# Kernel optimization log

Measured on AMD Instinct MI355X. Metric: run time of the kernel, lower is better.

Reference implementation:

```python
import jax, jax.numpy as jnp
import numpy as np

D_MODEL = 1024
N_HEADS = 16
D_K = D_MODEL // N_HEADS
B, S = 2, 2048


def setup_inputs() -> dict:
    key = jax.random.key(0)
    ks = jax.random.split(key, 5)
    x = jax.random.normal(ks[0], (B, S, D_MODEL), dtype=jnp.float32)
    # causal 0/1 mask, broadcastable over batch and heads
    mask = jnp.tril(jnp.ones((S, S), dtype=jnp.int32))[None, None, :, :]
    scale = 1.0 / np.sqrt(D_MODEL)
    w_qkv_w = jax.random.normal(ks[1], (3 * D_MODEL, D_MODEL), dtype=jnp.float32) * scale
    w_qkv_b = jnp.zeros((3 * D_MODEL,), dtype=jnp.float32)
    w_o_w = jax.random.normal(ks[2], (D_MODEL, D_MODEL), dtype=jnp.float32) * scale
    w_o_b = jnp.zeros((D_MODEL,), dtype=jnp.float32)
    return {"x": x, "mask": mask, "w_qkv_w": w_qkv_w, "w_qkv_b": w_qkv_b,
            "w_o_w": w_o_w, "w_o_b": w_o_b}


def reference(x, mask, w_qkv_w, w_qkv_b, w_o_w, w_o_b):
    b, s, d = x.shape
    qkv = x @ w_qkv_w.T + w_qkv_b                       # [b, s, 3d]
    q, k, v = jnp.split(qkv, 3, axis=-1)
    # [b, h, s, dk]
    q = q.reshape(b, s, N_HEADS, D_K).transpose(0, 2, 1, 3)
    k = k.reshape(b, s, N_HEADS, D_K).transpose(0, 2, 1, 3)
    v = v.reshape(b, s, N_HEADS, D_K).transpose(0, 2, 1, 3)
    scores = jnp.einsum('bhqd,bhkd->bhqk', q, k) / jnp.sqrt(jnp.float32(D_K))
    scores = jnp.where(mask == 0, jnp.float32(-1e9), scores)
    attn = jax.nn.softmax(scores, axis=-1)
    out = jnp.einsum('bhqk,bhkd->bhqd', attn, v)        # [b, h, s, dk]
    out = out.transpose(0, 2, 1, 3).reshape(b, s, d)
    return out @ w_o_w.T + w_o_b
```

## Files before the change

### kernel.cpp

```cpp
#include <hip/hip_runtime.h>
#include <cstdint>
#include <cstddef>


typedef __attribute__((ext_vector_type(8))) short bf16x8;
typedef __attribute__((ext_vector_type(4))) float f32x4;
typedef __attribute__((ext_vector_type(4))) unsigned int u32x4;
typedef __attribute__((ext_vector_type(4))) unsigned short u16x4;
typedef __attribute__((ext_vector_type(8))) unsigned short u16x8;

__device__ __forceinline__ unsigned short f2b(float f) {
  unsigned int u = __float_as_uint(f);
  u = u + 0x7FFFu + ((u >> 16) & 1u);
  return (unsigned short)(u >> 16);
}
__device__ __forceinline__ unsigned short f2b_trunc(float f) {
  return (unsigned short)(__float_as_uint(f) >> 16);
}

__device__ __forceinline__ void gl_lds16(const unsigned short* g, unsigned short* s) {
  __builtin_amdgcn_global_load_lds((const __attribute__((address_space(1))) void*)g,
                                   (__attribute__((address_space(3))) void*)s, 16, 0, 0);
}

__global__ __launch_bounds__(256) void cvt_all(const float* __restrict__ x,
                                               const float* __restrict__ wq,
                                               const float* __restrict__ wo,
                                               unsigned short* __restrict__ xb,
                                               unsigned short* __restrict__ wqb,
                                               unsigned short* __restrict__ wob) {
  const int bid = blockIdx.x;
  const float* in;
  unsigned short* out;
  int base;
  if (bid < 4096)      { in = x;  out = xb;  base = bid; }
  else if (bid < 7168) { in = wq; out = wqb; base = bid - 4096; }
  else                 { in = wo; out = wob; base = bid - 7168; }
  const int idx = (base * 256 + threadIdx.x) * 4;
  f32x4 v = *(const f32x4*)(in + idx);
  u16x4 r;
  r[0] = f2b(v[0]); r[1] = f2b(v[1]); r[2] = f2b(v[2]); r[3] = f2b(v[3]);
  *(u16x4*)(out + idx) = r;
}

__global__ __launch_bounds__(256) void gemm_bt(const unsigned short* __restrict__ A,
                                               const unsigned short* __restrict__ W,
                                               const float* __restrict__ bias,
                                               unsigned short* __restrict__ Cb,
                                               int M, int N, int K, int qcols) {
  __shared__ unsigned short As[2][128 * 32];
  __shared__ unsigned short Bs[2][128 * 32];
  const int tid  = threadIdx.x;
  const int lane = tid & 63;
  const int w    = tid >> 6;
  const int wy   = w >> 1, wx = w & 1;
  const int l15  = lane & 15, quad = lane >> 4;
  const int xr2  = (l15 >> 1) & 3;
  const int m0 = blockIdx.y * 128, n0 = blockIdx.x * 128;

  const unsigned short* gA[2];
  const unsigned short* gB[2];
  int off[2];
#pragma unroll
  for (int p = 0; p < 2; ++p) {
    const int c = tid + p * 256;
    const int r = c >> 2;
    const int srcc = (c & 3) ^ ((r >> 1) & 3);
    gA[p] = A + (size_t)(m0 + r) * K + srcc * 8;
    gB[p] = W + (size_t)(n0 + r) * K + srcc * 8;
    off[p] = c * 8;
  }

  f32x4 acc[4][4];
#pragma unroll
  for (int i = 0; i < 4; ++i)
#pragma unroll
    for (int j = 0; j < 4; ++j) acc[i][j] = (f32x4){0.f, 0.f, 0.f, 0.f};

#pragma unroll
  for (int p = 0; p < 2; ++p) {
    gl_lds16(gA[p], &As[0][off[p]]);
    gl_lds16(gB[p], &Bs[0][off[p]]);
  }

  const int NIT = K >> 5;
  for (int it = 0; it < NIT; ++it) {
    __syncthreads();
    const int cur = it & 1;
    if (it + 1 < NIT) {
      const int kt = (it + 1) << 5;
#pragma unroll
      for (int p = 0; p < 2; ++p) {
        gl_lds16(gA[p] + kt, &As[cur ^ 1][off[p]]);
        gl_lds16(gB[p] + kt, &Bs[cur ^ 1][off[p]]);
      }
    }
    const unsigned short* Ac = As[cur];
    const unsigned short* Bc = Bs[cur];
    bf16x8 af[4], bfr[4];
#pragma unroll
    for (int i = 0; i < 4; ++i)
      af[i] = *(const bf16x8*)&Ac[(wy * 64 + i * 16 + l15) * 32 + (quad ^ xr2) * 8];
#pragma unroll
    for (int j = 0; j < 4; ++j)
      bfr[j] = *(const bf16x8*)&Bc[(wx * 64 + j * 16 + l15) * 32 + (quad ^ xr2) * 8];
#pragma unroll
    for (int i = 0; i < 4; ++i)
#pragma unroll
      for (int j = 0; j < 4; ++j)
        acc[i][j] = __builtin_amdgcn_mfma_f32_16x16x32_bf16(af[i], bfr[j], acc[i][j], 0, 0, 0);
  }

#pragma unroll
  for (int i = 0; i < 4; ++i) {
    const int row = m0 + wy * 64 + i * 16 + quad * 4;
#pragma unroll
    for (int j = 0; j < 4; ++j) {
      const int col = n0 + wx * 64 + j * 16 + l15;
      const float bv = bias[col];
      const float sc = (col < qcols) ? 0.125f : 1.0f;
#pragma unroll
      for (int r = 0; r < 4; ++r)
        Cb[(size_t)(row + r) * N + col] = f2b((acc[i][j][r] + bv) * sc);
    }
  }
}

__global__ __launch_bounds__(256) void gemm_bt64(const unsigned short* __restrict__ A,
                                                 const unsigned short* __restrict__ W,
                                                 const float* __restrict__ bias,
                                                 float* __restrict__ Cf,
                                                 int M, int N, int K) {
  __shared__ unsigned short As[2][64 * 32];
  __shared__ unsigned short Bs[2][128 * 32];
  const int tid  = threadIdx.x;
  const int lane = tid & 63;
  const int w    = tid >> 6;
  const int wy   = w >> 1, wx = w & 1;
  const int l15  = lane & 15, quad = lane >> 4;
  const int xr2  = (l15 >> 1) & 3;
  const int m0 = blockIdx.y * 64, n0 = blockIdx.x * 128;

  const unsigned short* gA0;
  int offA0;
  {
    const int c = tid;
    const int r = c >> 2;
    const int srcc = (c & 3) ^ ((r >> 1) & 3);
    gA0 = A + (size_t)(m0 + r) * K + srcc * 8;
    offA0 = c * 8;
  }
  const unsigned short* gB[2];
  int offB[2];
#pragma unroll
  for (int p = 0; p < 2; ++p) {
    const int c = tid + p * 256;
    const int r = c >> 2;
    const int srcc = (c & 3) ^ ((r >> 1) & 3);
    gB[p] = W + (size_t)(n0 + r) * K + srcc * 8;
    offB[p] = c * 8;
  }

  f32x4 acc[2][4];
#pragma unroll
  for (int i = 0; i < 2; ++i)
#pragma unroll
    for (int j = 0; j < 4; ++j) acc[i][j] = (f32x4){0.f, 0.f, 0.f, 0.f};

  gl_lds16(gA0, &As[0][offA0]);
#pragma unroll
  for (int p = 0; p < 2; ++p) gl_lds16(gB[p], &Bs[0][offB[p]]);

  const int NIT = K >> 5;
  for (int it = 0; it < NIT; ++it) {
    __syncthreads();
    const int cur = it & 1;
    if (it + 1 < NIT) {
      const int kt = (it + 1) << 5;
      gl_lds16(gA0 + kt, &As[cur ^ 1][offA0]);
#pragma unroll
      for (int p = 0; p < 2; ++p) gl_lds16(gB[p] + kt, &Bs[cur ^ 1][offB[p]]);
    }
    const unsigned short* Ac = As[cur];
    const unsigned short* Bc = Bs[cur];
    bf16x8 af[2], bfr[4];
#pragma unroll
    for (int i = 0; i < 2; ++i)
      af[i] = *(const bf16x8*)&Ac[(wy * 32 + i * 16 + l15) * 32 + (quad ^ xr2) * 8];
#pragma unroll
    for (int j = 0; j < 4; ++j)
      bfr[j] = *(const bf16x8*)&Bc[(wx * 64 + j * 16 + l15) * 32 + (quad ^ xr2) * 8];
#pragma unroll
    for (int i = 0; i < 2; ++i)
#pragma unroll
      for (int j = 0; j < 4; ++j)
        acc[i][j] = __builtin_amdgcn_mfma_f32_16x16x32_bf16(af[i], bfr[j], acc[i][j], 0, 0, 0);
  }

#pragma unroll
  for (int i = 0; i < 2; ++i) {
    const int row = m0 + wy * 32 + i * 16 + quad * 4;
#pragma unroll
    for (int j = 0; j < 4; ++j) {
      const int col = n0 + wx * 64 + j * 16 + l15;
      const float bv = bias[col];
#pragma unroll
      for (int r = 0; r < 4; ++r)
        Cf[(size_t)(row + r) * N + col] = acc[i][j][r] + bv;
    }
  }
}

__global__ __launch_bounds__(256) void transpose_v(const unsigned short* __restrict__ qkv,
                                                   unsigned short* __restrict__ vt) {
  __shared__ unsigned short tile[64][72];
  const int tid = threadIdx.x;
  const int bh = blockIdx.y, b = bh >> 4, h = bh & 15;
  const int s0 = blockIdx.x * 64;
  const int i = tid >> 2;
  const int j = (tid & 3) * 16;
  const unsigned short* g = qkv + (size_t)(b * 2048 + s0 + i) * 3072 + 2048 + h * 64 + j;
  *(u32x4*)&tile[i][j]     = *(const u32x4*)g;
  *(u32x4*)&tile[i][j + 8] = *(const u32x4*)(g + 8);
  __syncthreads();
  const int d  = tid >> 2;
  const int sj = (tid & 3) * 16;
  u16x8 o0, o1;
#pragma unroll
  for (int k = 0; k < 8; ++k) { o0[k] = tile[sj + k][d]; o1[k] = tile[sj + 8 + k][d]; }
  unsigned short* gout = vt + (size_t)(bh * 64 + d) * 2048 + s0 + sj;
  *(u16x8*)gout       = o0;
  *(u16x8*)(gout + 8) = o1;
}

__global__ __launch_bounds__(256, 3) void attn_fwd(const unsigned short* __restrict__ qkv,
                                                   const unsigned short* __restrict__ vt,
                                                   unsigned short* __restrict__ o) {
  __shared__ unsigned short Ks[2][64 * 72];
  __shared__ unsigned short Vs[2][64 * 72];
  __shared__ unsigned short pbuf[4][16 * 72];
  const int tid  = threadIdx.x;
  const int lane = tid & 63;
  const int w    = tid >> 6;
  const int l15  = lane & 15, quad = lane >> 4;
  const int bh = blockIdx.x, b = bh >> 4, h = bh & 15;
  const int qt = 15 - (int)blockIdx.y;
  const int q0 = qt * 128;
  const int qa = q0 + w * 32;
  const int qb = qa + 16;
  const int T = 2 * qt + 2;

  const int srow = tid >> 2;
  const int scol = (tid & 3) * 16;
  const unsigned short* gK = qkv + (size_t)(b * 2048 + srow) * 3072 + 1024 + h * 64 + scol;
  const unsigned short* gV = vt + (size_t)(bh * 64 + srow) * 2048 + scol;

  const unsigned short* qra = qkv + (size_t)(b * 2048 + qa + l15) * 3072 + h * 64;
  const unsigned short* qrb = qkv + (size_t)(b * 2048 + qb + l15) * 3072 + h * 64;
  const bf16x8 bq[2][2] = {
    { *(const bf16x8*)(qra + quad * 8), *(const bf16x8*)(qra + 32 + quad * 8) },
    { *(const bf16x8*)(qrb + quad * 8), *(const bf16x8*)(qrb + 32 + quad * 8) } };

  bf16x8 vones;
#pragma unroll
  for (int k = 0; k < 8; ++k) vones[k] = (short)0x3F80;

  f32x4 acc[2][4];
#pragma unroll
  for (int i = 0; i < 2; ++i)
#pragma unroll
    for (int j = 0; j < 4; ++j) acc[i][j] = (f32x4){0.f, 0.f, 0.f, 0.f};
  f32x4 accL[2] = {(f32x4){0.f, 0.f, 0.f, 0.f}, (f32x4){0.f, 0.f, 0.f, 0.f}};

  unsigned short* P = pbuf[w];

  {
    u32x4 k0 = *(const u32x4*)gK, k1 = *(const u32x4*)(gK + 8);
    u32x4 v0 = *(const u32x4*)gV, v1 = *(const u32x4*)(gV + 8);
    unsigned short* sK = &Ks[0][srow * 72 + scol];
    unsigned short* sV = &Vs[0][srow * 72 + scol];
    *(u32x4*)sK = k0; *(u32x4*)(sK + 8) = k1;
    *(u32x4*)sV = v0; *(u32x4*)(sV + 8) = v1;
  }

  for (int t = 0; t < T; ++t) {
    __syncthreads();
    const int cur = t & 1;
    const unsigned short* Kc = Ks[cur];
    const unsigned short* Vc = Vs[cur];
    u32x4 nk0, nk1, nv0, nv1;
    const bool more = (t + 1 < T);
    if (more) {
      const size_t ko = (size_t)(t + 1) * 64 * 3072;
      const int vo = (t + 1) * 64;
      nk0 = *(const u32x4*)(gK + ko); nk1 = *(const u32x4*)(gK + ko + 8);
      nv0 = *(const u32x4*)(gV + vo); nv1 = *(const u32x4*)(gV + vo + 8);
    }
    const int kv0 = t * 64;

    f32x4 st[2][4];
#pragma unroll
    for (int n = 0; n < 4; ++n) {
      const bf16x8 kA0 = *(const bf16x8*)&Kc[(n * 16 + l15) * 72 + quad * 8];
      const bf16x8 kA1 = *(const bf16x8*)&Kc[(n * 16 + l15) * 72 + 32 + quad * 8];
      f32x4 z0 = (f32x4){0.f, 0.f, 0.f, 0.f};
      z0 = __builtin_amdgcn_mfma_f32_16x16x32_bf16(kA0, bq[0][0], z0, 0, 0, 0);
      z0 = __builtin_amdgcn_mfma_f32_16x16x32_bf16(kA1, bq[0][1], z0, 0, 0, 0);
      st[0][n] = z0;
      f32x4 z1 = (f32x4){0.f, 0.f, 0.f, 0.f};
      z1 = __builtin_amdgcn_mfma_f32_16x16x32_bf16(kA0, bq[1][0], z1, 0, 0, 0);
      z1 = __builtin_amdgcn_mfma_f32_16x16x32_bf16(kA1, bq[1][1], z1, 0, 0, 0);
      st[1][n] = z1;
    }
    bf16x8 av[4][2];
#pragma unroll
    for (int j = 0; j < 4; ++j) {
      av[j][0] = *(const bf16x8*)&Vc[(j * 16 + l15) * 72 + quad * 8];
      av[j][1] = *(const bf16x8*)&Vc[(j * 16 + l15) * 72 + 32 + quad * 8];
    }
#pragma unroll
    for (int tq = 0; tq < 2; ++tq) {
      const int qbase = tq ? qb : qa;
      if (kv0 + 63 > qbase) {
        const int qrow = qbase + l15;
#pragma unroll
        for (int n = 0; n < 4; ++n)
#pragma unroll
          for (int r = 0; r < 4; ++r)
            if (kv0 + n * 16 + quad * 4 + r > qrow) st[tq][n][r] = -1e30f;
      }
#pragma unroll
      for (int n = 0; n < 4; ++n) {
#pragma unroll
        for (int r = 0; r < 4; ++r) st[tq][n][r] = __expf(st[tq][n][r]);
        u16x4 pw;
        pw[0] = f2b_trunc(st[tq][n][0]); pw[1] = f2b_trunc(st[tq][n][1]);
        pw[2] = f2b_trunc(st[tq][n][2]); pw[3] = f2b_trunc(st[tq][n][3]);
        *(u16x4*)&P[l15 * 72 + n * 16 + quad * 4] = pw;
      }
      const bf16x8 bp0 = *(const bf16x8*)&P[l15 * 72 + quad * 8];
      const bf16x8 bp1 = *(const bf16x8*)&P[l15 * 72 + 32 + quad * 8];
      accL[tq] = __builtin_amdgcn_mfma_f32_16x16x32_bf16(vones, bp0, accL[tq], 0, 0, 0);
      accL[tq] = __builtin_amdgcn_mfma_f32_16x16x32_bf16(vones, bp1, accL[tq], 0, 0, 0);
#pragma unroll
      for (int j = 0; j < 4; ++j) {
        acc[tq][j] = __builtin_amdgcn_mfma_f32_16x16x32_bf16(av[j][0], bp0, acc[tq][j], 0, 0, 0);
        acc[tq][j] = __builtin_amdgcn_mfma_f32_16x16x32_bf16(av[j][1], bp1, acc[tq][j], 0, 0, 0);
      }
    }
    if (more) {
      unsigned short* sK = &Ks[cur ^ 1][srow * 72 + scol];
      unsigned short* sV = &Vs[cur ^ 1][srow * 72 + scol];
      *(u32x4*)sK = nk0; *(u32x4*)(sK + 8) = nk1;
      *(u32x4*)sV = nv0; *(u32x4*)(sV + 8) = nv1;
    }
  }
#pragma unroll
  for (int tq = 0; tq < 2; ++tq) {
    const int qrow = (tq ? qb : qa) + l15;
    const float inv = 1.0f / accL[tq][0];
    unsigned short* orow = o + (size_t)(b * 2048 + qrow) * 1024 + h * 64;
#pragma unroll
    for (int j = 0; j < 4; ++j) {
      u16x4 ov;
      ov[0] = f2b(acc[tq][j][0] * inv); ov[1] = f2b(acc[tq][j][1] * inv);
      ov[2] = f2b(acc[tq][j][2] * inv); ov[3] = f2b(acc[tq][j][3] * inv);
      *(u16x4*)(orow + j * 16 + quad * 4) = ov;
    }
  }
}

extern "C" void kernel_launch(void* const* d_in, const int* in_sizes, int n_in,
                              void* d_out, int out_size, void* d_ws, size_t ws_size,
                              hipStream_t stream) {
  const float* x       = (const float*)d_in[0];
  const float* w_qkv_w = (const float*)d_in[2];
  const float* w_qkv_b = (const float*)d_in[3];
  const float* w_o_w   = (const float*)d_in[4];
  const float* w_o_b   = (const float*)d_in[5];
  float* out = (float*)d_out;

  unsigned short* ws    = (unsigned short*)d_ws;
  unsigned short* xb    = ws;
  unsigned short* wqb   = xb   + (size_t)4096 * 1024;
  unsigned short* wob   = wqb  + (size_t)3072 * 1024;
  unsigned short* qkvb  = wob  + (size_t)1024 * 1024;
  unsigned short* vtb   = qkvb + (size_t)4096 * 3072;
  unsigned short* attnb = vtb  + (size_t)2048 * 2048;

  cvt_all<<<8192, 256, 0, stream>>>(x, w_qkv_w, w_o_w, xb, wqb, wob);
  gemm_bt<<<dim3(24, 32), 256, 0, stream>>>(xb, wqb, w_qkv_b, qkvb, 4096, 3072, 1024, 1024);
  transpose_v<<<dim3(32, 32), 256, 0, stream>>>(qkvb, vtb);
  attn_fwd<<<dim3(32, 16), 256, 0, stream>>>(qkvb, vtb, attnb);
  gemm_bt64<<<dim3(8, 64), 256, 0, stream>>>(attnb, wob, w_o_b, out, 4096, 1024, 1024);
}
```

Measured before the change: 196.3 us.

## Halve attention and output GEMM tile sizes, load V directly from global

The attention kernel now gives each block 64 query rows (16 per wave) instead of 128, doubling the grid to 1024 blocks and raising the occupancy hint to 4. V fragments are read straight from global memory each iteration instead of being staged through double-buffered LDS, which frees LDS and registers. The output-projection GEMM tile shrinks from 64x128 to 64x64 to double its block count. The goal is better CU utilisation and load balance across the causal triangle, at the cost of less K reuse per block and uncached-through-LDS global V loads sitting on the critical path.

```diff
diff --git a/kernel.cpp b/kernel.cpp
--- a/kernel.cpp
+++ b/kernel.cpp
@@ -132,44 +132,35 @@
                                                  float* __restrict__ Cf,
                                                  int M, int N, int K) {
   __shared__ unsigned short As[2][64 * 32];
-  __shared__ unsigned short Bs[2][128 * 32];
+  __shared__ unsigned short Bs[2][64 * 32];
   const int tid  = threadIdx.x;
   const int lane = tid & 63;
   const int w    = tid >> 6;
   const int wy   = w >> 1, wx = w & 1;
   const int l15  = lane & 15, quad = lane >> 4;
   const int xr2  = (l15 >> 1) & 3;
-  const int m0 = blockIdx.y * 64, n0 = blockIdx.x * 128;
+  const int m0 = blockIdx.y * 64, n0 = blockIdx.x * 64;
 
   const unsigned short* gA0;
-  int offA0;
+  const unsigned short* gB0;
+  int off0;
   {
     const int c = tid;
     const int r = c >> 2;
     const int srcc = (c & 3) ^ ((r >> 1) & 3);
     gA0 = A + (size_t)(m0 + r) * K + srcc * 8;
-    offA0 = c * 8;
-  }
-  const unsigned short* gB[2];
-  int offB[2];
-#pragma unroll
-  for (int p = 0; p < 2; ++p) {
-    const int c = tid + p * 256;
-    const int r = c >> 2;
-    const int srcc = (c & 3) ^ ((r >> 1) & 3);
-    gB[p] = W + (size_t)(n0 + r) * K + srcc * 8;
-    offB[p] = c * 8;
-  }
-
-  f32x4 acc[2][4];
+    gB0 = W + (size_t)(n0 + r) * K + srcc * 8;
+    off0 = c * 8;
+  }
+
+  f32x4 acc[2][2];
 #pragma unroll
   for (int i = 0; i < 2; ++i)
 #pragma unroll
-    for (int j = 0; j < 4; ++j) acc[i][j] = (f32x4){0.f, 0.f, 0.f, 0.f};
-
-  gl_lds16(gA0, &As[0][offA0]);
-#pragma unroll
-  for (int p = 0; p < 2; ++p) gl_lds16(gB[p], &Bs[0][offB[p]]);
+    for (int j = 0; j < 2; ++j) acc[i][j] = (f32x4){0.f, 0.f, 0.f, 0.f};
+
+  gl_lds16(gA0, &As[0][off0]);
+  gl_lds16(gB0, &Bs[0][off0]);
 
   const int NIT = K >> 5;
   for (int it = 0; it < NIT; ++it) {
@@ -177,23 +168,22 @@
     const int cur = it & 1;
     if (it + 1 < NIT) {
       const int kt = (it + 1) << 5;
-      gl_lds16(gA0 + kt, &As[cur ^ 1][offA0]);
-#pragma unroll
-      for (int p = 0; p < 2; ++p) gl_lds16(gB[p] + kt, &Bs[cur ^ 1][offB[p]]);
+      gl_lds16(gA0 + kt, &As[cur ^ 1][off0]);
+      gl_lds16(gB0 + kt, &Bs[cur ^ 1][off0]);
     }
     const unsigned short* Ac = As[cur];
     const unsigned short* Bc = Bs[cur];
-    bf16x8 af[2], bfr[4];
+    bf16x8 af[2], bfr[2];
 #pragma unroll
     for (int i = 0; i < 2; ++i)
       af[i] = *(const bf16x8*)&Ac[(wy * 32 + i * 16 + l15) * 32 + (quad ^ xr2) * 8];
 #pragma unroll
-    for (int j = 0; j < 4; ++j)
-      bfr[j] = *(const bf16x8*)&Bc[(wx * 64 + j * 16 + l15) * 32 + (quad ^ xr2) * 8];
+    for (int j = 0; j < 2; ++j)
+      bfr[j] = *(const bf16x8*)&Bc[(wx * 32 + j * 16 + l15) * 32 + (quad ^ xr2) * 8];
 #pragma unroll
     for (int i = 0; i < 2; ++i)
 #pragma unroll
-      for (int j = 0; j < 4; ++j)
+      for (int j = 0; j < 2; ++j)
         acc[i][j] = __builtin_amdgcn_mfma_f32_16x16x32_bf16(af[i], bfr[j], acc[i][j], 0, 0, 0);
   }
 
@@ -201,8 +191,8 @@
   for (int i = 0; i < 2; ++i) {
     const int row = m0 + wy * 32 + i * 16 + quad * 4;
 #pragma unroll
-    for (int j = 0; j < 4; ++j) {
-      const int col = n0 + wx * 64 + j * 16 + l15;
+    for (int j = 0; j < 2; ++j) {
+      const int col = n0 + wx * 32 + j * 16 + l15;
       const float bv = bias[col];
 #pragma unroll
       for (int r = 0; r < 4; ++r)
@@ -233,140 +223,114 @@
   *(u16x8*)(gout + 8) = o1;
 }
 
-__global__ __launch_bounds__(256, 3) void attn_fwd(const unsigned short* __restrict__ qkv,
+__global__ __launch_bounds__(256, 4) void attn_fwd(const unsigned short* __restrict__ qkv,
                                                    const unsigned short* __restrict__ vt,
                                                    unsigned short* __restrict__ o) {
   __shared__ unsigned short Ks[2][64 * 72];
-  __shared__ unsigned short Vs[2][64 * 72];
   __shared__ unsigned short pbuf[4][16 * 72];
   const int tid  = threadIdx.x;
   const int lane = tid & 63;
   const int w    = tid >> 6;
   const int l15  = lane & 15, quad = lane >> 4;
   const int bh = blockIdx.x, b = bh >> 4, h = bh & 15;
-  const int qt = 15 - (int)blockIdx.y;
-  const int q0 = qt * 128;
-  const int qa = q0 + w * 32;
-  const int qb = qa + 16;
-  const int T = 2 * qt + 2;
+  const int qt = 31 - (int)blockIdx.y;
+  const int q0 = qt * 64 + w * 16;
+  const int T = qt + 1;
 
   const int srow = tid >> 2;
   const int scol = (tid & 3) * 16;
   const unsigned short* gK = qkv + (size_t)(b * 2048 + srow) * 3072 + 1024 + h * 64 + scol;
-  const unsigned short* gV = vt + (size_t)(bh * 64 + srow) * 2048 + scol;
-
-  const unsigned short* qra = qkv + (size_t)(b * 2048 + qa + l15) * 3072 + h * 64;
-  const unsigned short* qrb = qkv + (size_t)(b * 2048 + qb + l15) * 3072 + h * 64;
-  const bf16x8 bq[2][2] = {
-    { *(const bf16x8*)(qra + quad * 8), *(const bf16x8*)(qra + 32 + quad * 8) },
-    { *(const bf16x8*)(qrb + quad * 8), *(const bf16x8*)(qrb + 32 + quad * 8) } };
+  const unsigned short* gV = vt + (size_t)(bh * 64) * 2048;
+
+  const unsigned short* qr = qkv + (size_t)(b * 2048 + q0 + l15) * 3072 + h * 64;
+  const bf16x8 bq0 = *(const bf16x8*)(qr + quad * 8);
+  const bf16x8 bq1 = *(const bf16x8*)(qr + 32 + quad * 8);
 
   bf16x8 vones;
 #pragma unroll
   for (int k = 0; k < 8; ++k) vones[k] = (short)0x3F80;
 
-  f32x4 acc[2][4];
-#pragma unroll
-  for (int i = 0; i < 2; ++i)
-#pragma unroll
-    for (int j = 0; j < 4; ++j) acc[i][j] = (f32x4){0.f, 0.f, 0.f, 0.f};
-  f32x4 accL[2] = {(f32x4){0.f, 0.f, 0.f, 0.f}, (f32x4){0.f, 0.f, 0.f, 0.f}};
+  f32x4 acc[4];
+#pragma unroll
+  for (int j = 0; j < 4; ++j) acc[j] = (f32x4){0.f, 0.f, 0.f, 0.f};
+  f32x4 accL = (f32x4){0.f, 0.f, 0.f, 0.f};
 
   unsigned short* P = pbuf[w];
 
   {
     u32x4 k0 = *(const u32x4*)gK, k1 = *(const u32x4*)(gK + 8);
-    u32x4 v0 = *(const u32x4*)gV, v1 = *(const u32x4*)(gV + 8);
     unsigned short* sK = &Ks[0][srow * 72 + scol];
-    unsigned short* sV = &Vs[0][srow * 72 + scol];
     *(u32x4*)sK = k0; *(u32x4*)(sK + 8) = k1;
-    *(u32x4*)sV = v0; *(u32x4*)(sV + 8) = v1;
   }
 
   for (int t = 0; t < T; ++t) {
     __syncthreads();
     const int cur = t & 1;
     const unsigned short* Kc = Ks[cur];
-    const unsigned short* Vc = Vs[cur];
-    u32x4 nk0, nk1, nv0, nv1;
+    const int kv0 = t * 64;
+    bf16x8 av[4][2];
+#pragma unroll
+    for (int j = 0; j < 4; ++j) {
+      const unsigned short* vrow = gV + (size_t)(j * 16 + l15) * 2048 + kv0;
+      av[j][0] = *(const bf16x8*)(vrow + quad * 8);
+      av[j][1] = *(const bf16x8*)(vrow + 32 + quad * 8);
+    }
+    u32x4 nk0, nk1;
     const bool more = (t + 1 < T);
     if (more) {
       const size_t ko = (size_t)(t + 1) * 64 * 3072;
-      const int vo = (t + 1) * 64;
       nk0 = *(const u32x4*)(gK + ko); nk1 = *(const u32x4*)(gK + ko + 8);
-      nv0 = *(const u32x4*)(gV + vo); nv1 = *(const u32x4*)(gV + vo + 8);
-    }
-    const int kv0 = t * 64;
-
-    f32x4 st[2][4];
+    }
+    f32x4 st[4];
 #pragma unroll
     for (int n = 0; n < 4; ++n) {
       const bf16x8 kA0 = *(const bf16x8*)&Kc[(n * 16 + l15) * 72 + quad * 8];
       const bf16x8 kA1 = *(const bf16x8*)&Kc[(n * 16 + l15) * 72 + 32 + quad * 8];
-      f32x4 z0 = (f32x4){0.f, 0.f, 0.f, 0.f};
-      z0 = __builtin_amdgcn_mfma_f32_16x16x32_bf16(kA0, bq[0][0], z0, 0, 0, 0);
-      z0 = __builtin_amdgcn_mfma_f32_16x16x32_bf16(kA1, bq[0][1], z0, 0, 0, 0);
-      st[0][n] = z0;
-      f32x4 z1 = (f32x4){0.f, 0.f, 0.f, 0.f};
-      z1 = __builtin_amdgcn_mfma_f32_16x16x32_bf16(kA0, bq[1][0], z1, 0, 0, 0);
-      z1 = __builtin_amdgcn_mfma_f32_16x16x32_bf16(kA1, bq[1][1], z1, 0, 0, 0);
-      st[1][n] = z1;
-    }
-    bf16x8 av[4][2];
+      f32x4 z = (f32x4){0.f, 0.f, 0.f, 0.f};
+      z = __builtin_amdgcn_mfma_f32_16x16x32_bf16(kA0, bq0, z, 0, 0, 0);
+      z = __builtin_amdgcn_mfma_f32_16x16x32_bf16(kA1, bq1, z, 0, 0, 0);
+      st[n] = z;
+    }
+    if (kv0 + 63 > q0) {
+      const int qrow = q0 + l15;
+#pragma unroll
+      for (int n = 0; n < 4; ++n)
+#pragma unroll
+        for (int r = 0; r < 4; ++r)
+          if (kv0 + n * 16 + quad * 4 + r > qrow) st[n][r] = -1e30f;
+    }
+#pragma unroll
+    for (int n = 0; n < 4; ++n) {
+#pragma unroll
+      for (int r = 0; r < 4; ++r) st[n][r] = __expf(st[n][r]);
+      u16x4 pw;
+      pw[0] = f2b_trunc(st[n][0]); pw[1] = f2b_trunc(st[n][1]);
+      pw[2] = f2b_trunc(st[n][2]); pw[3] = f2b_trunc(st[n][3]);
+      *(u16x4*)&P[l15 * 72 + n * 16 + quad * 4] = pw;
+    }
+    const bf16x8 bp0 = *(const bf16x8*)&P[l15 * 72 + quad * 8];
+    const bf16x8 bp1 = *(const bf16x8*)&P[l15 * 72 + 32 + quad * 8];
+    accL = __builtin_amdgcn_mfma_f32_16x16x32_bf16(vones, bp0, accL, 0, 0, 0);
+    accL = __builtin_amdgcn_mfma_f32_16x16x32_bf16(vones, bp1, accL, 0, 0, 0);
 #pragma unroll
     for (int j = 0; j < 4; ++j) {
-      av[j][0] = *(const bf16x8*)&Vc[(j * 16 + l15) * 72 + quad * 8];
-      av[j][1] = *(const bf16x8*)&Vc[(j * 16 + l15) * 72 + 32 + quad * 8];
-    }
-#pragma unroll
-    for (int tq = 0; tq < 2; ++tq) {
-      const int qbase = tq ? qb : qa;
-      if (kv0 + 63 > qbase) {
-        const int qrow = qbase + l15;
-#pragma unroll
-        for (int n = 0; n < 4; ++n)
-#pragma unroll
-          for (int r = 0; r < 4; ++r)
-            if (kv0 + n * 16 + quad * 4 + r > qrow) st[tq][n][r] = -1e30f;
-      }
-#pragma unroll
-      for (int n = 0; n < 4; ++n) {
-#pragma unroll
-        for (int r = 0; r < 4; ++r) st[tq][n][r] = __expf(st[tq][n][r]);
-        u16x4 pw;
-        pw[0] = f2b_trunc(st[tq][n][0]); pw[1] = f2b_trunc(st[tq][n][1]);
-        pw[2] = f2b_trunc(st[tq][n][2]); pw[3] = f2b_trunc(st[tq][n][3]);
-        *(u16x4*)&P[l15 * 72 + n * 16 + quad * 4] = pw;
-      }
-      const bf16x8 bp0 = *(const bf16x8*)&P[l15 * 72 + quad * 8];
-      const bf16x8 bp1 = *(const bf16x8*)&P[l15 * 72 + 32 + quad * 8];
-      accL[tq] = __builtin_amdgcn_mfma_f32_16x16x32_bf16(vones, bp0, accL[tq], 0, 0, 0);
-      accL[tq] = __builtin_amdgcn_mfma_f32_16x16x32_bf16(vones, bp1, accL[tq], 0, 0, 0);
-#pragma unroll
-      for (int j = 0; j < 4; ++j) {
-        acc[tq][j] = __builtin_amdgcn_mfma_f32_16x16x32_bf16(av[j][0], bp0, acc[tq][j], 0, 0, 0);
-        acc[tq][j] = __builtin_amdgcn_mfma_f32_16x16x32_bf16(av[j][1], bp1, acc[tq][j], 0, 0, 0);
-      }
+      acc[j] = __builtin_amdgcn_mfma_f32_16x16x32_bf16(av[j][0], bp0, acc[j], 0, 0, 0);
+      acc[j] = __builtin_amdgcn_mfma_f32_16x16x32_bf16(av[j][1], bp1, acc[j], 0, 0, 0);
     }
     if (more) {
       unsigned short* sK = &Ks[cur ^ 1][srow * 72 + scol];
-      unsigned short* sV = &Vs[cur ^ 1][srow * 72 + scol];
       *(u32x4*)sK = nk0; *(u32x4*)(sK + 8) = nk1;
-      *(u32x4*)sV = nv0; *(u32x4*)(sV + 8) = nv1;
-    }
-  }
-#pragma unroll
-  for (int tq = 0; tq < 2; ++tq) {
-    const int qrow = (tq ? qb : qa) + l15;
-    const float inv = 1.0f / accL[tq][0];
-    unsigned short* orow = o + (size_t)(b * 2048 + qrow) * 1024 + h * 64;
-#pragma unroll
-    for (int j = 0; j < 4; ++j) {
-      u16x4 ov;
-      ov[0] = f2b(acc[tq][j][0] * inv); ov[1] = f2b(acc[tq][j][1] * inv);
-      ov[2] = f2b(acc[tq][j][2] * inv); ov[3] = f2b(acc[tq][j][3] * inv);
-      *(u16x4*)(orow + j * 16 + quad * 4) = ov;
-    }
+    }
+  }
+  const int qrow = q0 + l15;
+  const float inv = 1.0f / accL[0];
+  unsigned short* orow = o + (size_t)(b * 2048 + qrow) * 1024 + h * 64;
+#pragma unroll
+  for (int j = 0; j < 4; ++j) {
+    u16x4 ov;
+    ov[0] = f2b(acc[j][0] * inv); ov[1] = f2b(acc[j][1] * inv);
+    ov[2] = f2b(acc[j][2] * inv); ov[3] = f2b(acc[j][3] * inv);
+    *(u16x4*)(orow + j * 16 + quad * 4) = ov;
   }
 }
 
@@ -391,6 +355,6 @@
   cvt_all<<<8192, 256, 0, stream>>>(x, w_qkv_w, w_o_w, xb, wqb, wob);
   gemm_bt<<<dim3(24, 32), 256, 0, stream>>>(xb, wqb, w_qkv_b, qkvb, 4096, 3072, 1024, 1024);
   transpose_v<<<dim3(32, 32), 256, 0, stream>>>(qkvb, vtb);
-  attn_fwd<<<dim3(32, 16), 256, 0, stream>>>(qkvb, vtb, attnb);
-  gemm_bt64<<<dim3(8, 64), 256, 0, stream>>>(attnb, wob, w_o_b, out, 4096, 1024, 1024);
-}
+  attn_fwd<<<dim3(32, 32), 256, 0, stream>>>(qkvb, vtb, attnb);
+  gemm_bt64<<<dim3(16, 64), 256, 0, stream>>>(attnb, wob, w_o_b, out, 4096, 1024, 1024);
+}
```

New measurement: 232.5 us. +18.5%, slower.

## Fuse V transpose into QKV GEMM epilogue and shrink output GEMM tiles

Applied to the files above, without the earlier changes.

The QKV projection GEMM now writes V columns straight into the transposed vt layout, so the separate transpose_v kernel and its extra read and write of V are gone. Each lane stores four consecutive sequence positions as one 8-byte vector into the transposed buffer. The output projection GEMM moves from 64x128 to 64x64 tiles, doubling the grid to 1024 blocks for better CU occupancy, at the cost of less data reuse per block. The transposed V stores are narrower and more scattered than before.

```diff
diff --git a/kernel.cpp b/kernel.cpp
--- a/kernel.cpp
+++ b/kernel.cpp
@@ -47,6 +47,7 @@
                                                const unsigned short* __restrict__ W,
                                                const float* __restrict__ bias,
                                                unsigned short* __restrict__ Cb,
+                                               unsigned short* __restrict__ vtb,
                                                int M, int N, int K, int qcols) {
   __shared__ unsigned short As[2][128 * 32];
   __shared__ unsigned short Bs[2][128 * 32];
@@ -111,6 +112,7 @@
         acc[i][j] = __builtin_amdgcn_mfma_f32_16x16x32_bf16(af[i], bfr[j], acc[i][j], 0, 0, 0);
   }
 
+  const bool vblock = (n0 >= 2048);
 #pragma unroll
   for (int i = 0; i < 4; ++i) {
     const int row = m0 + wy * 64 + i * 16 + quad * 4;
@@ -118,10 +120,19 @@
     for (int j = 0; j < 4; ++j) {
       const int col = n0 + wx * 64 + j * 16 + l15;
       const float bv = bias[col];
-      const float sc = (col < qcols) ? 0.125f : 1.0f;
-#pragma unroll
-      for (int r = 0; r < 4; ++r)
-        Cb[(size_t)(row + r) * N + col] = f2b((acc[i][j][r] + bv) * sc);
+      if (!vblock) {
+        const float sc = (col < qcols) ? 0.125f : 1.0f;
+#pragma unroll
+        for (int r = 0; r < 4; ++r)
+          Cb[(size_t)(row + r) * N + col] = f2b((acc[i][j][r] + bv) * sc);
+      } else {
+        const int hd = col - 2048;
+        const int bb = row >> 11, s = row & 2047;
+        u16x4 ov;
+#pragma unroll
+        for (int r = 0; r < 4; ++r) ov[r] = f2b(acc[i][j][r] + bv);
+        *(u16x4*)(vtb + ((size_t)(bb * 1024 + hd)) * 2048 + s) = ov;
+      }
     }
   }
 }
@@ -132,44 +143,35 @@
                                                  float* __restrict__ Cf,
                                                  int M, int N, int K) {
   __shared__ unsigned short As[2][64 * 32];
-  __shared__ unsigned short Bs[2][128 * 32];
+  __shared__ unsigned short Bs[2][64 * 32];
   const int tid  = threadIdx.x;
   const int lane = tid & 63;
   const int w    = tid >> 6;
   const int wy   = w >> 1, wx = w & 1;
   const int l15  = lane & 15, quad = lane >> 4;
   const int xr2  = (l15 >> 1) & 3;
-  const int m0 = blockIdx.y * 64, n0 = blockIdx.x * 128;
+  const int m0 = blockIdx.y * 64, n0 = blockIdx.x * 64;
 
   const unsigned short* gA0;
-  int offA0;
+  const unsigned short* gB0;
+  int off0;
   {
     const int c = tid;
     const int r = c >> 2;
     const int srcc = (c & 3) ^ ((r >> 1) & 3);
     gA0 = A + (size_t)(m0 + r) * K + srcc * 8;
-    offA0 = c * 8;
-  }
-  const unsigned short* gB[2];
-  int offB[2];
-#pragma unroll
-  for (int p = 0; p < 2; ++p) {
-    const int c = tid + p * 256;
-    const int r = c >> 2;
-    const int srcc = (c & 3) ^ ((r >> 1) & 3);
-    gB[p] = W + (size_t)(n0 + r) * K + srcc * 8;
-    offB[p] = c * 8;
-  }
-
-  f32x4 acc[2][4];
+    gB0 = W + (size_t)(n0 + r) * K + srcc * 8;
+    off0 = c * 8;
+  }
+
+  f32x4 acc[2][2];
 #pragma unroll
   for (int i = 0; i < 2; ++i)
 #pragma unroll
-    for (int j = 0; j < 4; ++j) acc[i][j] = (f32x4){0.f, 0.f, 0.f, 0.f};
-
-  gl_lds16(gA0, &As[0][offA0]);
-#pragma unroll
-  for (int p = 0; p < 2; ++p) gl_lds16(gB[p], &Bs[0][offB[p]]);
+    for (int j = 0; j < 2; ++j) acc[i][j] = (f32x4){0.f, 0.f, 0.f, 0.f};
+
+  gl_lds16(gA0, &As[0][off0]);
+  gl_lds16(gB0, &Bs[0][off0]);
 
   const int NIT = K >> 5;
   for (int it = 0; it < NIT; ++it) {
@@ -177,23 +179,22 @@
     const int cur = it & 1;
     if (it + 1 < NIT) {
       const int kt = (it + 1) << 5;
-      gl_lds16(gA0 + kt, &As[cur ^ 1][offA0]);
-#pragma unroll
-      for (int p = 0; p < 2; ++p) gl_lds16(gB[p] + kt, &Bs[cur ^ 1][offB[p]]);
+      gl_lds16(gA0 + kt, &As[cur ^ 1][off0]);
+      gl_lds16(gB0 + kt, &Bs[cur ^ 1][off0]);
     }
     const unsigned short* Ac = As[cur];
     const unsigned short* Bc = Bs[cur];
-    bf16x8 af[2], bfr[4];
+    bf16x8 af[2], bfr[2];
 #pragma unroll
     for (int i = 0; i < 2; ++i)
       af[i] = *(const bf16x8*)&Ac[(wy * 32 + i * 16 + l15) * 32 + (quad ^ xr2) * 8];
 #pragma unroll
-    for (int j = 0; j < 4; ++j)
-      bfr[j] = *(const bf16x8*)&Bc[(wx * 64 + j * 16 + l15) * 32 + (quad ^ xr2) * 8];
+    for (int j = 0; j < 2; ++j)
+      bfr[j] = *(const bf16x8*)&Bc[(wx * 32 + j * 16 + l15) * 32 + (quad ^ xr2) * 8];
 #pragma unroll
     for (int i = 0; i < 2; ++i)
 #pragma unroll
-      for (int j = 0; j < 4; ++j)
+      for (int j = 0; j < 2; ++j)
         acc[i][j] = __builtin_amdgcn_mfma_f32_16x16x32_bf16(af[i], bfr[j], acc[i][j], 0, 0, 0);
   }
 
@@ -201,36 +202,14 @@
   for (int i = 0; i < 2; ++i) {
     const int row = m0 + wy * 32 + i * 16 + quad * 4;
 #pragma unroll
-    for (int j = 0; j < 4; ++j) {
-      const int col = n0 + wx * 64 + j * 16 + l15;
+    for (int j = 0; j < 2; ++j) {
+      const int col = n0 + wx * 32 + j * 16 + l15;
       const float bv = bias[col];
 #pragma unroll
       for (int r = 0; r < 4; ++r)
         Cf[(size_t)(row + r) * N + col] = acc[i][j][r] + bv;
     }
   }
-}
-
-__global__ __launch_bounds__(256) void transpose_v(const unsigned short* __restrict__ qkv,
-                                                   unsigned short* __restrict__ vt) {
-  __shared__ unsigned short tile[64][72];
-  const int tid = threadIdx.x;
-  const int bh = blockIdx.y, b = bh >> 4, h = bh & 15;
-  const int s0 = blockIdx.x * 64;
-  const int i = tid >> 2;
-  const int j = (tid & 3) * 16;
-  const unsigned short* g = qkv + (size_t)(b * 2048 + s0 + i) * 3072 + 2048 + h * 64 + j;
-  *(u32x4*)&tile[i][j]     = *(const u32x4*)g;
-  *(u32x4*)&tile[i][j + 8] = *(const u32x4*)(g + 8);
-  __syncthreads();
-  const int d  = tid >> 2;
-  const int sj = (tid & 3) * 16;
-  u16x8 o0, o1;
-#pragma unroll
-  for (int k = 0; k < 8; ++k) { o0[k] = tile[sj + k][d]; o1[k] = tile[sj + 8 + k][d]; }
-  unsigned short* gout = vt + (size_t)(bh * 64 + d) * 2048 + s0 + sj;
-  *(u16x8*)gout       = o0;
-  *(u16x8*)(gout + 8) = o1;
 }
 
 __global__ __launch_bounds__(256, 3) void attn_fwd(const unsigned short* __restrict__ qkv,
@@ -389,8 +368,7 @@
   unsigned short* attnb = vtb  + (size_t)2048 * 2048;
 
   cvt_all<<<8192, 256, 0, stream>>>(x, w_qkv_w, w_o_w, xb, wqb, wob);
-  gemm_bt<<<dim3(24, 32), 256, 0, stream>>>(xb, wqb, w_qkv_b, qkvb, 4096, 3072, 1024, 1024);
-  transpose_v<<<dim3(32, 32), 256, 0, stream>>>(qkvb, vtb);
+  gemm_bt<<<dim3(24, 32), 256, 0, stream>>>(xb, wqb, w_qkv_b, qkvb, vtb, 4096, 3072, 1024, 1024);
   attn_fwd<<<dim3(32, 16), 256, 0, stream>>>(qkvb, vtb, attnb);
-  gemm_bt64<<<dim3(8, 64), 256, 0, stream>>>(attnb, wob, w_o_b, out, 4096, 1024, 1024);
-}
+  gemm_bt64<<<dim3(16, 64), 256, 0, stream>>>(attnb, wob, w_o_b, out, 4096, 1024, 1024);
+}
```

After: 190.8 us. 1.03x faster.
